# Kernel tuning notes

Hardware: AMD Instinct MI355X
Metric: run time of the kernel (lower is better)

The kernel has to match this reference:

```python
import jax, jax.numpy as jnp
import numpy as np

K = 3
STRIDE = 1
PADDING = 1


def _conv2d(x, w, b, stride, padding):
    out = jax.lax.conv_general_dilated(
        x, w, window_strides=(stride, stride),
        padding=[(padding, padding), (padding, padding)],
        dimension_numbers=('NCHW', 'OIHW', 'NCHW'))
    return out + b[None, :, None, None]


def _grid_sample_bilinear_zeros(x, grid):
    B, C, Hin, Win = x.shape
    gx = (grid[..., 0] + 1.0) * (Win * 0.5) - 0.5  # (B,Hg,Wg) pixel coords
    gy = (grid[..., 1] + 1.0) * (Hin * 0.5) - 0.5
    x0f = jnp.floor(gx)
    y0f = jnp.floor(gy)
    wx1 = gx - x0f  # bilinear weights
    wy1 = gy - y0f
    x0 = x0f.astype(jnp.int32)
    y0 = y0f.astype(jnp.int32)
    xf = x.reshape(B, C, Hin * Win)

    def gather(yi, xi):
        valid = (xi >= 0) & (xi < Win) & (yi >= 0) & (yi < Hin)  # zero padding
        idx = jnp.clip(yi, 0, Hin - 1) * Win + jnp.clip(xi, 0, Win - 1)
        g = jax.vmap(lambda xb, ib: xb[:, ib])(xf, idx)  # (B,C,Hg,Wg)
        return g * valid[:, None, :, :].astype(x.dtype)

    w00 = ((1.0 - wx1) * (1.0 - wy1))[:, None]
    w01 = (wx1 * (1.0 - wy1))[:, None]
    w10 = ((1.0 - wx1) * wy1)[:, None]
    w11 = (wx1 * wy1)[:, None]
    return (gather(y0, x0) * w00 + gather(y0, x0 + 1) * w01 +
            gather(y0 + 1, x0) * w10 + gather(y0 + 1, x0 + 1) * w11)


def setup_inputs() -> dict:
    key = jax.random.key(0)
    k1, k2, k3 = jax.random.split(key, 3)
    B, C, O, H, W = 8, 128, 128, 64, 64
    x = jax.random.normal(k1, (B, C, H, W), dtype=jnp.float32)
    # small offset-predictor weights so sampled locations stay near the grid
    w_off = jax.random.normal(k2, (2 * K * K, C, K, K), dtype=jnp.float32) * 1e-3
    b_off = jnp.zeros((2 * K * K,), dtype=jnp.float32)
    w_main = jax.random.normal(k3, (O, C, K, K), dtype=jnp.float32) * 0.05
    b_main = jnp.zeros((O,), dtype=jnp.float32)
    return {"x": x, "w_off": w_off, "b_off": b_off, "w_main": w_main, "b_main": b_main}


def reference(x, w_off, b_off, w_main, b_main):
    offset = _conv2d(x, w_off, b_off, STRIDE, PADDING)  # (B, 2*K*K, H, W)
    B, _, H, W = offset.shape
    off = jnp.transpose(offset, (0, 2, 3, 1)).reshape(B, H, W, K, K, 2)
    # The torch in-place loops reduce to:
    #   x-comp: cumsum over i of column j=0, broadcast over j
    #   y-comp: cumsum over j of row    i=0, broadcast over i
    ox = jnp.cumsum(off[:, :, :, :, 0, 0], axis=3)  # (B,H,W,K)
    oy = jnp.cumsum(off[:, :, :, 0, :, 1], axis=3)  # (B,H,W,K)
    ox_f = jnp.broadcast_to(ox[..., None], (B, H, W, K, K))
    oy_f = jnp.broadcast_to(oy[:, :, :, None, :], (B, H, W, K, K))
    off_f = jnp.stack([ox_f, oy_f], axis=-1).reshape(B, H, W, K * K, 2)

    y_range = jnp.linspace(-1.0, 1.0, H, dtype=x.dtype)
    x_range = jnp.linspace(-1.0, 1.0, W, dtype=x.dtype)
    yg, xg = jnp.meshgrid(y_range, x_range, indexing='ij')
    base = jnp.stack((xg, yg), axis=-1)  # (H,W,2)
    grid = base[None, :, :, None, :] + off_f  # (B,H,W,K*K,2)
    grid = grid.reshape(B, H, W * K * K, 2)

    xs = _grid_sample_bilinear_zeros(x, grid)  # (B,C,H,W*K*K)
    C = x.shape[1]
    xs = xs.reshape(B, C, H, W, K * K)
    wm = w_main.reshape(w_main.shape[0], C, K * K)
    out = jnp.einsum('bchwk,ock->bohw', xs, wm)
    return out + b_main[None, :, None, None]
```

## Files before the change

kernel.cpp:

```cpp
#include <hip/hip_runtime.h>
#include <hip/hip_bf16.h>
#include <stdint.h>

typedef unsigned short u16;
typedef unsigned int u32;
typedef __attribute__((ext_vector_type(8))) short short8;
typedef __attribute__((ext_vector_type(4))) float float4v;

#define CH 128
#define OO 128
#define KD 1152
#define MPIX 32768
#define IMB 16

__device__ __forceinline__ u16 f2bf(float v) {
    __hip_bfloat16 h = __float2bfloat16(v);
    return *reinterpret_cast<u16*>(&h);
}

__device__ __forceinline__ float bf_lo(u32 u) {
    u32 t = u << 16;
    return __builtin_bit_cast(float, t);
}
__device__ __forceinline__ float bf_hi(u32 u) {
    u32 t = u & 0xffff0000u;
    return __builtin_bit_cast(float, t);
}
__device__ __forceinline__ u32 pack_bf16(float lo, float hi) {
    u32 ul = __builtin_bit_cast(u32, lo);
    u32 uh = __builtin_bit_cast(u32, hi);
    return ((ul + 0x8000u) >> 16) | ((uh + 0x8000u) & 0xffff0000u);
}

__global__ __launch_bounds__(256) void transpose_kernel(const float* __restrict__ x,
                                                        __hip_bfloat16* __restrict__ xt) {
    __shared__ float st[64][65];
    int tid = threadIdx.x;
    int bh = blockIdx.x;
    int b = bh >> 6;
    int h = bh & 63;
    const float* xb = x + ((size_t)b * CH) * 4096 + (size_t)h * 64;
    __hip_bfloat16* xo = xt + ((size_t)bh << 6) * CH;
    for (int cc0 = 0; cc0 < 128; cc0 += 64) {
        #pragma unroll
        for (int step = 0; step < 16; ++step) {
            int cl = (tid >> 6) + step * 4;
            int w = tid & 63;
            st[cl][w] = xb[(size_t)(cc0 + cl) * 4096 + w];
        }
        __syncthreads();
        #pragma unroll
        for (int step = 0; step < 16; ++step) {
            int w = (tid >> 6) + step * 4;
            int cl = tid & 63;
            xo[(size_t)w * CH + cc0 + cl] = __float2bfloat16(st[cl][w]);
        }
        __syncthreads();
    }
}

__global__ __launch_bounds__(256) void offset_conv_kernel(const float* __restrict__ x,
                                                          const float* __restrict__ w_off,
                                                          float* __restrict__ partial) {
    int tid = threadIdx.x;
    int m = blockIdx.x * 256 + tid;
    int chunk = blockIdx.y;
    int b = m >> 12;
    int hw = m & 4095;
    int h = hw >> 6;
    int w = hw & 63;
    float acc[6] = {0.f, 0.f, 0.f, 0.f, 0.f, 0.f};
    int c0 = chunk * 32;
    for (int c = c0; c < c0 + 32; ++c) {
        const float* xc = x + ((size_t)(b * CH + c) << 12);
        float xv[9];
        #pragma unroll
        for (int dy = 0; dy < 3; ++dy) {
            int yy = h + dy - 1;
            bool vy = (unsigned)yy < 64u;
            #pragma unroll
            for (int dx = 0; dx < 3; ++dx) {
                int xx = w + dx - 1;
                bool vv = vy && ((unsigned)xx < 64u);
                xv[dy * 3 + dx] = vv ? xc[yy * 64 + xx] : 0.f;
            }
        }
        const float* wb = w_off + (size_t)c * 9;
        #pragma unroll
        for (int s = 0; s < 6; ++s) {
            int chn = (s < 3) ? s * 6 : (s - 3) * 2 + 1;
            const float* wp = wb + (size_t)chn * (CH * 9);
            float a = acc[s];
            #pragma unroll
            for (int t = 0; t < 9; ++t) a = fmaf(xv[t], wp[t], a);
            acc[s] = a;
        }
    }
    float* po = partial + ((size_t)(chunk << 15) + m) * 6;
    #pragma unroll
    for (int s = 0; s < 6; ++s) po[s] = acc[s];
}

__global__ __launch_bounds__(256) void wreorder_kernel(const float* __restrict__ w_main,
                                                       u16* __restrict__ Wb) {
    int idx = blockIdx.x * 256 + threadIdx.x;
    if (idx >= OO * KD) return;
    int o = idx / KD;
    int r = idx - o * KD;
    int k = r >> 7;
    int c = r & 127;
    Wb[idx] = f2bf(w_main[(size_t)o * KD + c * 9 + k]);
}

__global__ __launch_bounds__(256) void im2col_kernel(const __hip_bfloat16* __restrict__ xt,
                                                     const float* __restrict__ partial,
                                                     const float* __restrict__ b_off,
                                                     u16* __restrict__ Apix) {
    __shared__ float offs[IMB][6];
    __shared__ float2 gxy[IMB][9];
    int tid = threadIdx.x;
    int m0 = blockIdx.x * IMB;
    int b = m0 >> 12;
    int h = (m0 & 4095) >> 6;
    int w0 = m0 & 63;

    if (tid < IMB * 6) {
        int pix = tid / 6, s = tid % 6;
        int m = m0 + pix;
        int chn = (s < 3) ? s * 6 : (s - 3) * 2 + 1;
        float v = b_off[chn];
        #pragma unroll
        for (int q = 0; q < 4; ++q) v += partial[((size_t)(q << 15) + m) * 6 + s];
        offs[pix][s] = v;
    }
    __syncthreads();
    if (tid < IMB * 9) {
        int pix = tid / 9, k = tid % 9;
        int i = k / 3, j = k - i * 3;
        float ox = offs[pix][0];
        if (i >= 1) ox += offs[pix][1];
        if (i >= 2) ox += offs[pix][2];
        float oy = offs[pix][3];
        if (j >= 1) oy += offs[pix][4];
        if (j >= 2) oy += offs[pix][5];
        const float step = 2.0f / 63.0f;
        float bxn = -1.0f + (w0 + pix) * step;
        float byn = -1.0f + h * step;
        gxy[pix][k] = make_float2(fmaf(bxn + ox, 32.0f, 31.5f),
                                  fmaf(byn + oy, 32.0f, 31.5f));
    }
    __syncthreads();

    int pix = tid >> 4;
    int c8 = (tid & 15) * 8;
    const u32* xb = (const u32*)(xt + (((size_t)b << 12) * CH));
    u16* ao = Apix + (size_t)(m0 + pix) * KD + c8;

    for (int k = 0; k < 9; ++k) {
        float2 g = gxy[pix][k];
        float x0f = floorf(g.x), y0f = floorf(g.y);
        float wx = g.x - x0f, wy = g.y - y0f;
        int ix0 = (int)x0f, iy0 = (int)y0f;
        int ix1 = ix0 + 1, iy1 = iy0 + 1;
        float fx0 = ((unsigned)ix0 < 64u) ? 1.f : 0.f;
        float fx1 = ((unsigned)ix1 < 64u) ? 1.f : 0.f;
        float fy0 = ((unsigned)iy0 < 64u) ? 1.f : 0.f;
        float fy1 = ((unsigned)iy1 < 64u) ? 1.f : 0.f;
        float w00 = (1.f - wy) * (1.f - wx) * fy0 * fx0;
        float w01 = (1.f - wy) * wx * fy0 * fx1;
        float w10 = wy * (1.f - wx) * fy1 * fx0;
        float w11 = wy * wx * fy1 * fx1;
        int cx0 = min(max(ix0, 0), 63), cx1 = min(max(ix1, 0), 63);
        int cy0 = min(max(iy0, 0), 63), cy1 = min(max(iy1, 0), 63);
        int base00 = ((cy0 * 64 + cx0) * CH + c8) >> 1;
        int base01 = ((cy0 * 64 + cx1) * CH + c8) >> 1;
        int base10 = ((cy1 * 64 + cx0) * CH + c8) >> 1;
        int base11 = ((cy1 * 64 + cx1) * CH + c8) >> 1;
        uint4 u00 = *(const uint4*)(xb + base00);
        uint4 u01 = *(const uint4*)(xb + base01);
        uint4 u10 = *(const uint4*)(xb + base10);
        uint4 u11 = *(const uint4*)(xb + base11);
        u32 outp[4];
        const u32* p00 = (const u32*)&u00;
        const u32* p01 = (const u32*)&u01;
        const u32* p10 = (const u32*)&u10;
        const u32* p11 = (const u32*)&u11;
        #pragma unroll
        for (int q = 0; q < 4; ++q) {
            float lo = w00 * bf_lo(p00[q]);
            lo = fmaf(w01, bf_lo(p01[q]), lo);
            lo = fmaf(w10, bf_lo(p10[q]), lo);
            lo = fmaf(w11, bf_lo(p11[q]), lo);
            float hi = w00 * bf_hi(p00[q]);
            hi = fmaf(w01, bf_hi(p01[q]), hi);
            hi = fmaf(w10, bf_hi(p10[q]), hi);
            hi = fmaf(w11, bf_hi(p11[q]), hi);
            outp[q] = pack_bf16(lo, hi);
        }
        *(uint4*)(ao + k * CH) = *(const uint4*)outp;
    }
}

__global__ __launch_bounds__(256) void gemm_kernel(const u16* __restrict__ Wb,
                                                   const u16* __restrict__ Apix,
                                                   const float* __restrict__ b_main,
                                                   float* __restrict__ out) {
    __shared__ __align__(16) u16 lA[64 * 32];
    __shared__ __align__(16) u16 lB[128 * 32];
    int tid = threadIdx.x;
    int wave = tid >> 6;
    int lane = tid & 63;
    int wmh = wave & 1;
    int wn = wave >> 1;
    int ob = blockIdx.y * 64;
    int pb = blockIdx.x * 128;
    int mrow = lane & 15;
    int q8 = (lane >> 4) * 8;

    float4v acc[2][4];
    #pragma unroll
    for (int sm = 0; sm < 2; ++sm)
        #pragma unroll
        for (int sn = 0; sn < 4; ++sn)
            acc[sm][sn] = (float4v){0.f, 0.f, 0.f, 0.f};

    const u16* Ap = Wb + (size_t)ob * KD;
    const u16* Bp = Apix + (size_t)pb * KD;

    int arow = tid >> 2;
    int acol = (tid & 3) * 8;
    int brow0 = tid >> 1;
    int bcol0 = (tid & 1) * 16;

    for (int kk = 0; kk < 36; ++kk) {
        int col0 = kk * 32;
        *(uint4*)&lA[(arow * 32) + acol] = *(const uint4*)(Ap + (size_t)arow * KD + col0 + acol);
        #pragma unroll
        for (int q = 0; q < 2; ++q) {
            int idx = q * 256 + tid;
            int row = idx >> 2;
            int cole = (idx & 3) * 8;
            *(uint4*)&lB[row * 32 + cole] = *(const uint4*)(Bp + (size_t)row * KD + col0 + cole);
        }
        __syncthreads();
        short8 af[2], bfv[4];
        #pragma unroll
        for (int s = 0; s < 2; ++s)
            af[s] = *(const short8*)&lA[(wmh * 32 + s * 16 + mrow) * 32 + q8];
        #pragma unroll
        for (int s = 0; s < 4; ++s)
            bfv[s] = *(const short8*)&lB[(wn * 64 + s * 16 + mrow) * 32 + q8];
        #pragma unroll
        for (int sm = 0; sm < 2; ++sm)
            #pragma unroll
            for (int sn = 0; sn < 4; ++sn)
                acc[sm][sn] = __builtin_amdgcn_mfma_f32_16x16x32_bf16(af[sm], bfv[sn],
                                                                     acc[sm][sn], 0, 0, 0);
        __syncthreads();
    }

    #pragma unroll
    for (int sm = 0; sm < 2; ++sm) {
        int o = ob + wmh * 32 + sm * 16 + (lane >> 4) * 4;
        #pragma unroll
        for (int sn = 0; sn < 4; ++sn) {
            int pcol = pb + wn * 64 + sn * 16 + mrow;
            int b = pcol >> 12;
            int rem = pcol & 4095;
            float* op = out + (((size_t)b * OO) << 12) + rem;
            #pragma unroll
            for (int r = 0; r < 4; ++r)
                op[(size_t)(o + r) << 12] = acc[sm][sn][r] + b_main[o + r];
        }
    }
}

extern "C" void kernel_launch(void* const* d_in, const int* in_sizes, int n_in,
                              void* d_out, int out_size, void* d_ws, size_t ws_size,
                              hipStream_t stream) {
    const float* x      = (const float*)d_in[0];
    const float* w_off  = (const float*)d_in[1];
    const float* b_off  = (const float*)d_in[2];
    const float* w_main = (const float*)d_in[3];
    const float* b_main = (const float*)d_in[4];
    float* out = (float*)d_out;

    char* ws = (char*)d_ws;
    __hip_bfloat16* xt = (__hip_bfloat16*)ws;
    float* partial = (float*)(ws + 8388608);
    u16* Wb   = (u16*)(ws + 8388608 + 3145728);
    u16* Apix = (u16*)(ws + 8388608 + 3145728 + 294912);

    transpose_kernel<<<512, 256, 0, stream>>>(x, xt);
    offset_conv_kernel<<<dim3(128, 4), 256, 0, stream>>>(x, w_off, partial);
    wreorder_kernel<<<576, 256, 0, stream>>>(w_main, Wb);
    im2col_kernel<<<MPIX / IMB, 256, 0, stream>>>(xt, partial, b_off, Apix);
    gemm_kernel<<<dim3(256, 2), 256, 0, stream>>>(Wb, Apix, b_main, out);
}
```

Before: 140.9 us.

## Fuse bilinear im2col sampling into the MFMA GEMM, dropping the Apix buffer

Replaces the separate im2col kernel and GEMM with one kernel. Each block computes sampling coordinates for 128 pixels, bilinearly gathers the bf16 inputs straight into shared memory per (tap, channel-half) slice, then runs MFMA over all 128 output channels. This removes the write and re-read of the 75 MB Apix intermediate and one launch. In exchange the grid shrinks to 256 blocks, there is no overlap between gather latency and MFMA, and larger per-thread accumulators raise register pressure.

Measured after the change: 171.6 us. 21.8% more time.

```diff
diff --git a/kernel.cpp b/kernel.cpp
--- a/kernel.cpp
+++ b/kernel.cpp
@@ -11,21 +11,14 @@
 #define OO 128
 #define KD 1152
 #define MPIX 32768
-#define IMB 16
+#define LDA 72
 
 __device__ __forceinline__ u16 f2bf(float v) {
     __hip_bfloat16 h = __float2bfloat16(v);
     return *reinterpret_cast<u16*>(&h);
 }
-
-__device__ __forceinline__ float bf_lo(u32 u) {
-    u32 t = u << 16;
-    return __builtin_bit_cast(float, t);
-}
-__device__ __forceinline__ float bf_hi(u32 u) {
-    u32 t = u & 0xffff0000u;
-    return __builtin_bit_cast(float, t);
-}
+__device__ __forceinline__ float bf_lo(u32 u) { u32 t = u << 16;        return __builtin_bit_cast(float, t); }
+__device__ __forceinline__ float bf_hi(u32 u) { u32 t = u & 0xffff0000u; return __builtin_bit_cast(float, t); }
 __device__ __forceinline__ u32 pack_bf16(float lo, float hi) {
     u32 ul = __builtin_bit_cast(u32, lo);
     u32 uh = __builtin_bit_cast(u32, hi);
@@ -112,156 +105,146 @@
     Wb[idx] = f2bf(w_main[(size_t)o * KD + c * 9 + k]);
 }
 
-__global__ __launch_bounds__(256) void im2col_kernel(const __hip_bfloat16* __restrict__ xt,
-                                                     const float* __restrict__ partial,
-                                                     const float* __restrict__ b_off,
-                                                     u16* __restrict__ Apix) {
-    __shared__ float offs[IMB][6];
-    __shared__ float2 gxy[IMB][9];
-    int tid = threadIdx.x;
-    int m0 = blockIdx.x * IMB;
-    int b = m0 >> 12;
-    int h = (m0 & 4095) >> 6;
-    int w0 = m0 & 63;
-
-    if (tid < IMB * 6) {
-        int pix = tid / 6, s = tid % 6;
-        int m = m0 + pix;
-        int chn = (s < 3) ? s * 6 : (s - 3) * 2 + 1;
-        float v = b_off[chn];
-        #pragma unroll
-        for (int q = 0; q < 4; ++q) v += partial[((size_t)(q << 15) + m) * 6 + s];
-        offs[pix][s] = v;
-    }
-    __syncthreads();
-    if (tid < IMB * 9) {
-        int pix = tid / 9, k = tid % 9;
-        int i = k / 3, j = k - i * 3;
-        float ox = offs[pix][0];
-        if (i >= 1) ox += offs[pix][1];
-        if (i >= 2) ox += offs[pix][2];
-        float oy = offs[pix][3];
-        if (j >= 1) oy += offs[pix][4];
-        if (j >= 2) oy += offs[pix][5];
-        const float step = 2.0f / 63.0f;
-        float bxn = -1.0f + (w0 + pix) * step;
-        float byn = -1.0f + h * step;
-        gxy[pix][k] = make_float2(fmaf(bxn + ox, 32.0f, 31.5f),
-                                  fmaf(byn + oy, 32.0f, 31.5f));
-    }
-    __syncthreads();
-
-    int pix = tid >> 4;
-    int c8 = (tid & 15) * 8;
-    const u32* xb = (const u32*)(xt + (((size_t)b << 12) * CH));
-    u16* ao = Apix + (size_t)(m0 + pix) * KD + c8;
-
-    for (int k = 0; k < 9; ++k) {
-        float2 g = gxy[pix][k];
-        float x0f = floorf(g.x), y0f = floorf(g.y);
-        float wx = g.x - x0f, wy = g.y - y0f;
-        int ix0 = (int)x0f, iy0 = (int)y0f;
-        int ix1 = ix0 + 1, iy1 = iy0 + 1;
-        float fx0 = ((unsigned)ix0 < 64u) ? 1.f : 0.f;
-        float fx1 = ((unsigned)ix1 < 64u) ? 1.f : 0.f;
-        float fy0 = ((unsigned)iy0 < 64u) ? 1.f : 0.f;
-        float fy1 = ((unsigned)iy1 < 64u) ? 1.f : 0.f;
-        float w00 = (1.f - wy) * (1.f - wx) * fy0 * fx0;
-        float w01 = (1.f - wy) * wx * fy0 * fx1;
-        float w10 = wy * (1.f - wx) * fy1 * fx0;
-        float w11 = wy * wx * fy1 * fx1;
-        int cx0 = min(max(ix0, 0), 63), cx1 = min(max(ix1, 0), 63);
-        int cy0 = min(max(iy0, 0), 63), cy1 = min(max(iy1, 0), 63);
-        int base00 = ((cy0 * 64 + cx0) * CH + c8) >> 1;
-        int base01 = ((cy0 * 64 + cx1) * CH + c8) >> 1;
-        int base10 = ((cy1 * 64 + cx0) * CH + c8) >> 1;
-        int base11 = ((cy1 * 64 + cx1) * CH + c8) >> 1;
-        uint4 u00 = *(const uint4*)(xb + base00);
-        uint4 u01 = *(const uint4*)(xb + base01);
-        uint4 u10 = *(const uint4*)(xb + base10);
-        uint4 u11 = *(const uint4*)(xb + base11);
-        u32 outp[4];
-        const u32* p00 = (const u32*)&u00;
-        const u32* p01 = (const u32*)&u01;
-        const u32* p10 = (const u32*)&u10;
-        const u32* p11 = (const u32*)&u11;
-        #pragma unroll
-        for (int q = 0; q < 4; ++q) {
-            float lo = w00 * bf_lo(p00[q]);
-            lo = fmaf(w01, bf_lo(p01[q]), lo);
-            lo = fmaf(w10, bf_lo(p10[q]), lo);
-            lo = fmaf(w11, bf_lo(p11[q]), lo);
-            float hi = w00 * bf_hi(p00[q]);
-            hi = fmaf(w01, bf_hi(p01[q]), hi);
-            hi = fmaf(w10, bf_hi(p10[q]), hi);
-            hi = fmaf(w11, bf_hi(p11[q]), hi);
-            outp[q] = pack_bf16(lo, hi);
-        }
-        *(uint4*)(ao + k * CH) = *(const uint4*)outp;
-    }
-}
-
-__global__ __launch_bounds__(256) void gemm_kernel(const u16* __restrict__ Wb,
-                                                   const u16* __restrict__ Apix,
-                                                   const float* __restrict__ b_main,
-                                                   float* __restrict__ out) {
-    __shared__ __align__(16) u16 lA[64 * 32];
-    __shared__ __align__(16) u16 lB[128 * 32];
+__global__ __launch_bounds__(256) void fused_gemm_kernel(const __hip_bfloat16* __restrict__ xt,
+                                                         const float* __restrict__ partial,
+                                                         const float* __restrict__ b_off,
+                                                         const u16* __restrict__ Wb,
+                                                         const float* __restrict__ b_main,
+                                                         float* __restrict__ out) {
+    __shared__ __align__(16) u16 lA[128 * LDA];
+    __shared__ __align__(16) u16 lB[128 * LDA];
+    __shared__ float2 gxy[128 * 9];
+
     int tid = threadIdx.x;
     int wave = tid >> 6;
     int lane = tid & 63;
-    int wmh = wave & 1;
+    int wm = wave & 1;
     int wn = wave >> 1;
-    int ob = blockIdx.y * 64;
-    int pb = blockIdx.x * 128;
     int mrow = lane & 15;
     int q8 = (lane >> 4) * 8;
-
-    float4v acc[2][4];
+    int pb = blockIdx.x * 128;
+    int bimg = pb >> 12;
+
+    float* offs = (float*)lB;
+    for (int idx = tid; idx < 128 * 6; idx += 256) {
+        int px = idx / 6, s = idx - px * 6;
+        int m = pb + px;
+        int chn = (s < 3) ? s * 6 : (s - 3) * 2 + 1;
+        float v = b_off[chn];
+        #pragma unroll
+        for (int q = 0; q < 4; ++q) v += partial[((size_t)(q << 15) + m) * 6 + s];
+        offs[idx] = v;
+    }
+    __syncthreads();
+    for (int idx = tid; idx < 128 * 9; idx += 256) {
+        int px = idx / 9, k = idx - px * 9;
+        int i = k / 3, j = k - i * 3;
+        float ox = offs[px * 6 + 0];
+        if (i >= 1) ox += offs[px * 6 + 1];
+        if (i >= 2) ox += offs[px * 6 + 2];
+        float oy = offs[px * 6 + 3];
+        if (j >= 1) oy += offs[px * 6 + 4];
+        if (j >= 2) oy += offs[px * 6 + 5];
+        int m = pb + px;
+        int h = (m & 4095) >> 6;
+        int w = m & 63;
+        const float step = 2.0f / 63.0f;
+        float bxn = -1.0f + w * step;
+        float byn = -1.0f + h * step;
+        gxy[idx] = make_float2(fmaf(bxn + ox, 32.0f, 31.5f),
+                               fmaf(byn + oy, 32.0f, 31.5f));
+    }
+    __syncthreads();
+
+    float4v acc[4][4];
     #pragma unroll
-    for (int sm = 0; sm < 2; ++sm)
+    for (int sm = 0; sm < 4; ++sm)
         #pragma unroll
         for (int sn = 0; sn < 4; ++sn)
             acc[sm][sn] = (float4v){0.f, 0.f, 0.f, 0.f};
 
-    const u16* Ap = Wb + (size_t)ob * KD;
-    const u16* Bp = Apix + (size_t)pb * KD;
-
-    int arow = tid >> 2;
-    int acol = (tid & 3) * 8;
-    int brow0 = tid >> 1;
-    int bcol0 = (tid & 1) * 16;
-
-    for (int kk = 0; kk < 36; ++kk) {
-        int col0 = kk * 32;
-        *(uint4*)&lA[(arow * 32) + acol] = *(const uint4*)(Ap + (size_t)arow * KD + col0 + acol);
-        #pragma unroll
-        for (int q = 0; q < 2; ++q) {
-            int idx = q * 256 + tid;
-            int row = idx >> 2;
-            int cole = (idx & 3) * 8;
-            *(uint4*)&lB[row * 32 + cole] = *(const uint4*)(Bp + (size_t)row * KD + col0 + cole);
-        }
-        __syncthreads();
-        short8 af[2], bfv[4];
-        #pragma unroll
-        for (int s = 0; s < 2; ++s)
-            af[s] = *(const short8*)&lA[(wmh * 32 + s * 16 + mrow) * 32 + q8];
-        #pragma unroll
-        for (int s = 0; s < 4; ++s)
-            bfv[s] = *(const short8*)&lB[(wn * 64 + s * 16 + mrow) * 32 + q8];
-        #pragma unroll
-        for (int sm = 0; sm < 2; ++sm)
+    const u32* xb = (const u32*)(xt + (((size_t)bimg << 12) * CH));
+
+    for (int ks = 0; ks < 18; ++ks) {
+        int k = ks >> 1;
+        int chalf = ks & 1;
+        #pragma unroll
+        for (int q = 0; q < 4; ++q) {
+            int unit = q * 256 + tid;
+            int o = unit >> 3, cg = unit & 7;
+            *(uint4*)&lA[o * LDA + cg * 8] =
+                *(const uint4*)(Wb + (size_t)o * KD + k * 128 + chalf * 64 + cg * 8);
+        }
+        #pragma unroll
+        for (int q = 0; q < 4; ++q) {
+            int unit = q * 256 + tid;
+            int px = unit >> 3, cg = unit & 7;
+            int c8 = chalf * 64 + cg * 8;
+            float2 g = gxy[px * 9 + k];
+            float x0f = floorf(g.x), y0f = floorf(g.y);
+            float wx = g.x - x0f, wy = g.y - y0f;
+            int ix0 = (int)x0f, iy0 = (int)y0f;
+            int ix1 = ix0 + 1, iy1 = iy0 + 1;
+            float fx0 = ((unsigned)ix0 < 64u) ? 1.f : 0.f;
+            float fx1 = ((unsigned)ix1 < 64u) ? 1.f : 0.f;
+            float fy0 = ((unsigned)iy0 < 64u) ? 1.f : 0.f;
+            float fy1 = ((unsigned)iy1 < 64u) ? 1.f : 0.f;
+            float w00 = (1.f - wy) * (1.f - wx) * fy0 * fx0;
+            float w01 = (1.f - wy) * wx * fy0 * fx1;
+            float w10 = wy * (1.f - wx) * fy1 * fx0;
+            float w11 = wy * wx * fy1 * fx1;
+            int cx0 = min(max(ix0, 0), 63), cx1 = min(max(ix1, 0), 63);
+            int cy0 = min(max(iy0, 0), 63), cy1 = min(max(iy1, 0), 63);
+            int base00 = ((cy0 * 64 + cx0) * CH + c8) >> 1;
+            int base01 = ((cy0 * 64 + cx1) * CH + c8) >> 1;
+            int base10 = ((cy1 * 64 + cx0) * CH + c8) >> 1;
+            int base11 = ((cy1 * 64 + cx1) * CH + c8) >> 1;
+            uint4 u00 = *(const uint4*)(xb + base00);
+            uint4 u01 = *(const uint4*)(xb + base01);
+            uint4 u10 = *(const uint4*)(xb + base10);
+            uint4 u11 = *(const uint4*)(xb + base11);
+            const u32* p00 = (const u32*)&u00;
+            const u32* p01 = (const u32*)&u01;
+            const u32* p10 = (const u32*)&u10;
+            const u32* p11 = (const u32*)&u11;
+            u32 outp[4];
+            #pragma unroll
+            for (int qq = 0; qq < 4; ++qq) {
+                float lo = w00 * bf_lo(p00[qq]);
+                lo = fmaf(w01, bf_lo(p01[qq]), lo);
+                lo = fmaf(w10, bf_lo(p10[qq]), lo);
+                lo = fmaf(w11, bf_lo(p11[qq]), lo);
+                float hi = w00 * bf_hi(p00[qq]);
+                hi = fmaf(w01, bf_hi(p01[qq]), hi);
+                hi = fmaf(w10, bf_hi(p10[qq]), hi);
+                hi = fmaf(w11, bf_hi(p11[qq]), hi);
+                outp[qq] = pack_bf16(lo, hi);
+            }
+            *(uint4*)&lB[px * LDA + cg * 8] = *(const uint4*)outp;
+        }
+        __syncthreads();
+        #pragma unroll
+        for (int s = 0; s < 2; ++s) {
+            short8 af[4], bfv[4];
+            #pragma unroll
+            for (int sm = 0; sm < 4; ++sm)
+                af[sm] = *(const short8*)&lA[(wm * 64 + sm * 16 + mrow) * LDA + s * 32 + q8];
             #pragma unroll
             for (int sn = 0; sn < 4; ++sn)
-                acc[sm][sn] = __builtin_amdgcn_mfma_f32_16x16x32_bf16(af[sm], bfv[sn],
-                                                                     acc[sm][sn], 0, 0, 0);
+                bfv[sn] = *(const short8*)&lB[(wn * 64 + sn * 16 + mrow) * LDA + s * 32 + q8];
+            #pragma unroll
+            for (int sm = 0; sm < 4; ++sm)
+                #pragma unroll
+                for (int sn = 0; sn < 4; ++sn)
+                    acc[sm][sn] = __builtin_amdgcn_mfma_f32_16x16x32_bf16(af[sm], bfv[sn],
+                                                                         acc[sm][sn], 0, 0, 0);
+        }
         __syncthreads();
     }
 
     #pragma unroll
-    for (int sm = 0; sm < 2; ++sm) {
-        int o = ob + wmh * 32 + sm * 16 + (lane >> 4) * 4;
+    for (int sm = 0; sm < 4; ++sm) {
+        int o = wm * 64 + sm * 16 + (lane >> 4) * 4;
         #pragma unroll
         for (int sn = 0; sn < 4; ++sn) {
             int pcol = pb + wn * 64 + sn * 16 + mrow;
@@ -289,11 +272,9 @@
     __hip_bfloat16* xt = (__hip_bfloat16*)ws;
     float* partial = (float*)(ws + 8388608);
     u16* Wb   = (u16*)(ws + 8388608 + 3145728);
-    u16* Apix = (u16*)(ws + 8388608 + 3145728 + 294912);
 
     transpose_kernel<<<512, 256, 0, stream>>>(x, xt);
     offset_conv_kernel<<<dim3(128, 4), 256, 0, stream>>>(x, w_off, partial);
     wreorder_kernel<<<576, 256, 0, stream>>>(w_main, Wb);
-    im2col_kernel<<<MPIX / IMB, 256, 0, stream>>>(xt, partial, b_off, Apix);
-    gemm_kernel<<<dim3(256, 2), 256, 0, stream>>>(Wb, Apix, b_main, out);
-}
+    fused_gemm_kernel<<<256, 256, 0, stream>>>(xt, partial, b_off, Wb, b_main, out);
+}
```
